# Kernel tuning notes

Measured on AMD Instinct MI355X. Metric: run time of the kernel, lower is better.

The kernel has to match this reference:

```python
import jax, jax.numpy as jnp
import numpy as np

B, T, C = 16, 2048, 1024
HEAD = 64

def setup_inputs() -> dict:
    key = jax.random.key(0)
    kx, kq, kk, kv = jax.random.split(key, 4)
    x = jax.random.normal(kx, (B, T, C), dtype=jnp.float32)
    s = 1.0 / np.sqrt(C)
    Wq = jax.random.normal(kq, (C, HEAD), dtype=jnp.float32) * s
    Wk = jax.random.normal(kk, (C, HEAD), dtype=jnp.float32) * s
    Wv = jax.random.normal(kv, (C, HEAD), dtype=jnp.float32) * s
    return {"x": x, "Wq": Wq, "Wk": Wk, "Wv": Wv}

def reference(x, Wq, Wk, Wv):
    Bb, Tt, Cc = x.shape
    q = jnp.einsum('btc,ch->bth', x, Wq)  # [B,T,H]
    k = jnp.einsum('btc,ch->bth', x, Wk)
    v = jnp.einsum('btc,ch->bth', x, Wv)
    # NOTE: source scales by C**-0.5 (n_embd), not head_size**-0.5
    scores = jnp.einsum('bth,bsh->bts', q, k) * (Cc ** -0.5)  # [B,T,T]
    causal = jnp.tril(jnp.ones((Tt, Tt), dtype=bool))
    scores = jnp.where(causal, scores, -jnp.inf)
    attn = jax.nn.softmax(scores, axis=-1)  # dropout p=0 -> identity
    out = jnp.einsum('bts,bsh->bth', attn, v)  # [B,T,H]
    return out
```

## Files before the change

kernel.cpp:

```cpp
#include <hip/hip_runtime.h>

typedef __bf16 bf16;
typedef __bf16 bf16x4 __attribute__((ext_vector_type(4)));
typedef __bf16 bf16x8 __attribute__((ext_vector_type(8)));
typedef float f32x4 __attribute__((ext_vector_type(4)));

#define TT_ 2048
#define CC_ 1024
#define HH_ 64

#define SCALE2 0.045084221f

__global__ __launch_bounds__(256) void prep_w(const float* __restrict__ Wq,
                                              const float* __restrict__ Wk,
                                              const float* __restrict__ Wv,
                                              bf16* __restrict__ Wt) {
    __shared__ bf16 Ls[64 * 65];
    const int m  = blockIdx.x >> 4;
    const int k0 = (blockIdx.x & 15) * 64;
    const float* W = (m == 0) ? Wq : (m == 1) ? Wk : Wv;
    const int tid = threadIdx.x;
    #pragma unroll
    for (int j = 0; j < 4; ++j) {
        int idx = tid + 256 * j;
        int r   = idx >> 4;
        int c4  = (idx & 15) * 4;
        float4 w = *(const float4*)&W[(size_t)(k0 + r) * HH_ + c4];
        Ls[r * 65 + c4 + 0] = (bf16)w.x;
        Ls[r * 65 + c4 + 1] = (bf16)w.y;
        Ls[r * 65 + c4 + 2] = (bf16)w.z;
        Ls[r * 65 + c4 + 3] = (bf16)w.w;
    }
    __syncthreads();
    #pragma unroll
    for (int j = 0; j < 4; ++j) {
        int idx = tid + 256 * j;
        int n   = idx >> 4;
        int kc  = (idx & 15) * 4;
        bf16x4 v;
        #pragma unroll
        for (int i = 0; i < 4; ++i) v[i] = Ls[(kc + i) * 65 + n];
        *(bf16x4*)&Wt[m * 65536 + n * 1024 + k0 + kc] = v;
    }
}

__global__ __launch_bounds__(256) void qkv_kernel(const float* __restrict__ x,
                                                  const bf16* __restrict__ Wt,
                                                  bf16* __restrict__ qb,
                                                  bf16* __restrict__ kb,
                                                  bf16* __restrict__ vt) {
    __shared__ __align__(16) bf16 Xs[2][64 * 72];
    const int tid  = threadIdx.x;
    const int wave = tid >> 6;
    const int lane = tid & 15;
    const int quad = (tid & 63) >> 4;
    const int m0   = blockIdx.x * 64;

    f32x4 acc[4][3];
    #pragma unroll
    for (int i = 0; i < 4; ++i)
        #pragma unroll
        for (int j = 0; j < 3; ++j) acc[i][j] = f32x4{0.f, 0.f, 0.f, 0.f};

    const int srow = tid >> 4;
    const int scol = (tid & 15) * 4;

    float4 xr[4];
    #pragma unroll
    for (int rr = 0; rr < 4; ++rr)
        xr[rr] = *(const float4*)&x[(size_t)(m0 + srow + rr * 16) * CC_ + scol];
    #pragma unroll
    for (int rr = 0; rr < 4; ++rr) {
        bf16x4 bv = {(bf16)xr[rr].x, (bf16)xr[rr].y, (bf16)xr[rr].z, (bf16)xr[rr].w};
        *(bf16x4*)&Xs[0][(srow + rr * 16) * 72 + scol] = bv;
    }

    for (int kbi = 0; kbi < 16; ++kbi) {
        const int cur = kbi & 1;
        const int k0  = kbi * 64;
        __syncthreads();
        if (kbi < 15) {
            #pragma unroll
            for (int rr = 0; rr < 4; ++rr)
                xr[rr] = *(const float4*)&x[(size_t)(m0 + srow + rr * 16) * CC_ + k0 + 64 + scol];
        }
        bf16x8 bfr[2][3];
        #pragma unroll
        for (int step = 0; step < 2; ++step)
            #pragma unroll
            for (int ct = 0; ct < 3; ++ct)
                bfr[step][ct] = *(const bf16x8*)&Wt[(size_t)(wave * 48 + ct * 16 + lane) * 1024 + k0 + step * 32 + quad * 8];
        bf16x8 afr[2][4];
        #pragma unroll
        for (int step = 0; step < 2; ++step)
            #pragma unroll
            for (int rt = 0; rt < 4; ++rt)
                afr[step][rt] = *(const bf16x8*)&Xs[cur][(rt * 16 + lane) * 72 + step * 32 + quad * 8];
        #pragma unroll
        for (int step = 0; step < 2; ++step)
            #pragma unroll
            for (int ct = 0; ct < 3; ++ct)
                #pragma unroll
                for (int rt = 0; rt < 4; ++rt)
                    acc[rt][ct] = __builtin_amdgcn_mfma_f32_16x16x32_bf16(afr[step][rt], bfr[step][ct], acc[rt][ct], 0, 0, 0);
        if (kbi < 15) {
            #pragma unroll
            for (int rr = 0; rr < 4; ++rr) {
                bf16x4 bv = {(bf16)xr[rr].x, (bf16)xr[rr].y, (bf16)xr[rr].z, (bf16)xr[rr].w};
                *(bf16x4*)&Xs[cur ^ 1][(srow + rr * 16) * 72 + scol] = bv;
            }
        }
    }

    const int bb = m0 >> 11;
    const int t0 = m0 & 2047;
    __syncthreads();
    #pragma unroll
    for (int ct = 0; ct < 3; ++ct) {
        int c0 = wave * 48 + ct * 16;
        if (c0 < 128) {
            bf16* outp = (c0 < 64) ? qb : kb;
            int h = (c0 & 63) + lane;
            #pragma unroll
            for (int rt = 0; rt < 4; ++rt)
                #pragma unroll
                for (int r = 0; r < 4; ++r)
                    outp[(size_t)(m0 + rt * 16 + quad * 4 + r) * HH_ + h] = (bf16)acc[rt][ct][r];
        } else {
            int h = (c0 - 128) + lane;
            #pragma unroll
            for (int rt = 0; rt < 4; ++rt)
                #pragma unroll
                for (int r = 0; r < 4; ++r)
                    Xs[0][(rt * 16 + quad * 4 + r) * 72 + h] = (bf16)acc[rt][ct][r];
        }
    }
    __syncthreads();
    {
        int h  = tid >> 2;
        int tc = (tid & 3) * 16;
        bf16x8 v0, v1;
        #pragma unroll
        for (int i = 0; i < 8; ++i) v0[i] = Xs[0][(tc + i) * 72 + h];
        #pragma unroll
        for (int i = 0; i < 8; ++i) v1[i] = Xs[0][(tc + 8 + i) * 72 + h];
        bf16* dst = &vt[(size_t)bb * HH_ * TT_ + (size_t)h * TT_ + t0 + tc];
        *(bf16x8*)dst = v0;
        *(bf16x8*)(dst + 8) = v1;
    }
}

__global__ __launch_bounds__(256) void attn_kernel(const bf16* __restrict__ qb,
                                                   const bf16* __restrict__ kb,
                                                   const bf16* __restrict__ vt,
                                                   bf16* __restrict__ PO,
                                                   float* __restrict__ PL) {
    __shared__ __align__(16) bf16 Ks[128 * 72];
    __shared__ __align__(16) bf16 Vs[64 * 136];
    __shared__ __align__(16) bf16 Ps[4][16 * 136];

    const int tid  = threadIdx.x;
    const int wave = tid >> 6;
    const int lane = tid & 15;
    const int quad = (tid & 63) >> 4;
    const int idx = blockIdx.x;
    const int bb  = blockIdx.y;
    int seg, qi;
    if (idx < 32)      { seg = 0; qi = idx; }
    else if (idx < 56) { seg = 1; qi = idx - 24; }
    else if (idx < 72) { seg = 2; qi = idx - 40; }
    else               { seg = 3; qi = idx - 48; }
    const int q0   = qi * 64;
    const int qrow = q0 + wave * 16;
    const int nch   = (seg < (qi >> 3)) ? 4 : (((qi & 7) + 2) >> 1);
    const int diagc = (seg == (qi >> 3)) ? nch - 1 : -1;

    bf16x8 aq[2];
    #pragma unroll
    for (int step = 0; step < 2; ++step)
        aq[step] = *(const bf16x8*)&qb[(size_t)(bb * TT_ + qrow + lane) * HH_ + step * 32 + quad * 8];

    f32x4 o_acc[4];
    #pragma unroll
    for (int ht = 0; ht < 4; ++ht) o_acc[ht] = f32x4{0.f, 0.f, 0.f, 0.f};
    float l_lane[4] = {0.f, 0.f, 0.f, 0.f};

    for (int c = 0; c < nch; ++c) {
        const int s0 = seg * 512 + c * 128;
        __syncthreads();
        #pragma unroll
        for (int j = 0; j < 4; ++j) {
            int ch = tid + 256 * j;
            int row = ch >> 3, c8 = (ch & 7) * 8;
            *(bf16x8*)&Ks[row * 72 + c8] =
                *(const bf16x8*)&kb[(size_t)(bb * TT_ + s0 + row) * HH_ + c8];
        }
        #pragma unroll
        for (int j = 0; j < 4; ++j) {
            int ch = tid + 256 * j;
            int h = ch >> 4, c8 = (ch & 15) * 8;
            *(bf16x8*)&Vs[h * 136 + c8] =
                *(const bf16x8*)&vt[(size_t)bb * HH_ * TT_ + (size_t)h * TT_ + s0 + c8];
        }
        __syncthreads();

        f32x4 sfr[8];
        #pragma unroll
        for (int nt = 0; nt < 8; ++nt) sfr[nt] = f32x4{0.f, 0.f, 0.f, 0.f};
        #pragma unroll
        for (int step = 0; step < 2; ++step)
            #pragma unroll
            for (int nt = 0; nt < 8; ++nt) {
                bf16x8 bk = *(const bf16x8*)&Ks[(nt * 16 + lane) * 72 + step * 32 + quad * 8];
                sfr[nt] = __builtin_amdgcn_mfma_f32_16x16x32_bf16(aq[step], bk, sfr[nt], 0, 0, 0);
            }

        const bool msk = (c == diagc);
        #pragma unroll
        for (int r = 0; r < 4; ++r) {
            const int rowg = qrow + quad * 4 + r;
            #pragma unroll
            for (int nt = 0; nt < 8; ++nt) {
                float e = __builtin_amdgcn_exp2f(sfr[nt][r] * SCALE2);
                if (msk && (s0 + nt * 16 + lane) > rowg) e = 0.f;
                sfr[nt][r] = e;
                l_lane[r] += e;
            }
        }

        #pragma unroll
        for (int nt = 0; nt < 8; ++nt)
            #pragma unroll
            for (int r = 0; r < 4; ++r)
                Ps[wave][(quad * 4 + r) * 136 + nt * 16 + lane] = (bf16)sfr[nt][r];

        #pragma unroll
        for (int step = 0; step < 4; ++step) {
            bf16x8 ap = *(const bf16x8*)&Ps[wave][lane * 136 + step * 32 + quad * 8];
            #pragma unroll
            for (int ht = 0; ht < 4; ++ht) {
                bf16x8 bv = *(const bf16x8*)&Vs[(ht * 16 + lane) * 136 + step * 32 + quad * 8];
                o_acc[ht] = __builtin_amdgcn_mfma_f32_16x16x32_bf16(ap, bv, o_acc[ht], 0, 0, 0);
            }
        }
    }

    const size_t p = (size_t)bb * 80 + idx;
    #pragma unroll
    for (int ht = 0; ht < 4; ++ht)
        #pragma unroll
        for (int r = 0; r < 4; ++r)
            PO[p * 4096 + (size_t)(wave * 16 + quad * 4 + r) * 64 + ht * 16 + lane] = (bf16)o_acc[ht][r];
    #pragma unroll
    for (int r = 0; r < 4; ++r) {
        float l = l_lane[r];
        l += __shfl_xor(l, 1);
        l += __shfl_xor(l, 2);
        l += __shfl_xor(l, 4);
        l += __shfl_xor(l, 8);
        if (lane == 0) PL[p * 64 + wave * 16 + quad * 4 + r] = l;
    }
}

__global__ __launch_bounds__(256) void combine_kernel(const bf16* __restrict__ PO,
                                                      const float* __restrict__ PL,
                                                      float* __restrict__ out) {
    const int qi = blockIdx.x, bb = blockIdx.y;
    const int tid = threadIdx.x;
    const int r  = tid >> 2;
    const int cb = (tid & 3) * 16;
    const int ns = (qi >> 3) + 1;
    const int off[4] = {0, 32, 56, 72};

    float acc[16];
    #pragma unroll
    for (int i = 0; i < 16; ++i) acc[i] = 0.f;
    float l = 0.f;
    for (int s = 0; s < ns; ++s) {
        const size_t p = (size_t)bb * 80 + off[s] + qi - 8 * s;
        l += PL[p * 64 + r];
        const bf16* po = &PO[p * 4096 + (size_t)r * 64 + cb];
        bf16x8 a0 = *(const bf16x8*)po;
        bf16x8 a1 = *(const bf16x8*)(po + 8);
        #pragma unroll
        for (int i = 0; i < 8; ++i) { acc[i] += (float)a0[i]; acc[8 + i] += (float)a1[i]; }
    }
    const float inv = 1.0f / l;
    float* dst = &out[(size_t)(bb * TT_ + qi * 64 + r) * HH_ + cb];
    #pragma unroll
    for (int v = 0; v < 4; ++v) {
        float4 o = {acc[v * 4] * inv, acc[v * 4 + 1] * inv, acc[v * 4 + 2] * inv, acc[v * 4 + 3] * inv};
        *(float4*)(dst + v * 4) = o;
    }
}

extern "C" void kernel_launch(void* const* d_in, const int* in_sizes, int n_in,
                              void* d_out, int out_size, void* d_ws, size_t ws_size,
                              hipStream_t stream) {
    const float* x  = (const float*)d_in[0];
    const float* Wq = (const float*)d_in[1];
    const float* Wk = (const float*)d_in[2];
    const float* Wv = (const float*)d_in[3];
    float* out = (float*)d_out;

    char* ws = (char*)d_ws;
    bf16*  qb = (bf16*)(ws);
    bf16*  kb = (bf16*)(ws + 4194304);
    bf16*  vt = (bf16*)(ws + 8388608);
    bf16*  Wt = (bf16*)(ws + 12582912);
    bf16*  PO = (bf16*)(ws + 12976128);
    float* PL = (float*)(ws + 23461888);

    prep_w<<<48, 256, 0, stream>>>(Wq, Wk, Wv, Wt);
    qkv_kernel<<<512, 256, 0, stream>>>(x, Wt, qb, kb, vt);
    attn_kernel<<<dim3(80, 16), 256, 0, stream>>>(qb, kb, vt, PO, PL);
    combine_kernel<<<dim3(32, 16), 256, 0, stream>>>(PO, PL, out);
}
```

Measured before the change: 259.8 us.

## Keep softmax probabilities in registers via transposed QK^T and 16x16x16 MFMA for PV

The attention kernel now computes S^T (K as the A operand, Q as B), so each lane's accumulator layout matches the A-operand layout of a 16x16x16 bf16 MFMA. The exponentiated scores can then feed the PV product directly from registers, with no Ps shared-memory round trip. K is read straight from global memory instead of being staged in LDS. V is double-buffered in LDS with register prefetch so there is one barrier per chunk, and fully masked diagonal sub-tiles are skipped. Risks are more global K traffic per wave, lower MFMA K-depth for PV, and the launch-bounds hint of 4 blocks per SM possibly constraining registers.

After: 272.1 us. 1.05x slower.

```diff
diff --git a/kernel.cpp b/kernel.cpp
--- a/kernel.cpp
+++ b/kernel.cpp
@@ -4,12 +4,27 @@
 typedef __bf16 bf16x4 __attribute__((ext_vector_type(4)));
 typedef __bf16 bf16x8 __attribute__((ext_vector_type(8)));
 typedef float f32x4 __attribute__((ext_vector_type(4)));
+typedef short short4v __attribute__((ext_vector_type(4)));
 
 #define TT_ 2048
 #define CC_ 1024
 #define HH_ 64
 
 #define SCALE2 0.045084221f
+
+static __device__ __forceinline__ f32x4 mfma16x16x16(bf16x4 a, bf16x4 b, f32x4 c) {
+#if __has_builtin(__builtin_amdgcn_mfma_f32_16x16x16_bf16)
+    return __builtin_amdgcn_mfma_f32_16x16x16_bf16(a, b, c, 0, 0, 0);
+#elif __has_builtin(__builtin_amdgcn_mfma_f32_16x16x16bf16_1k)
+    return __builtin_amdgcn_mfma_f32_16x16x16bf16_1k(__builtin_bit_cast(short4v, a),
+                                                     __builtin_bit_cast(short4v, b),
+                                                     c, 0, 0, 0);
+#else
+    f32x4 d;
+    asm("v_mfma_f32_16x16x16_bf16 %0, %1, %2, %3" : "=v"(d) : "v"(a), "v"(b), "v"(c));
+    return d;
+#endif
+}
 
 __global__ __launch_bounds__(256) void prep_w(const float* __restrict__ Wq,
                                               const float* __restrict__ Wk,
@@ -150,14 +165,12 @@
     }
 }
 
-__global__ __launch_bounds__(256) void attn_kernel(const bf16* __restrict__ qb,
-                                                   const bf16* __restrict__ kb,
-                                                   const bf16* __restrict__ vt,
-                                                   bf16* __restrict__ PO,
-                                                   float* __restrict__ PL) {
-    __shared__ __align__(16) bf16 Ks[128 * 72];
-    __shared__ __align__(16) bf16 Vs[64 * 136];
-    __shared__ __align__(16) bf16 Ps[4][16 * 136];
+__global__ __launch_bounds__(256, 4) void attn_kernel(const bf16* __restrict__ qb,
+                                                      const bf16* __restrict__ kb,
+                                                      const bf16* __restrict__ vt,
+                                                      bf16* __restrict__ PO,
+                                                      float* __restrict__ PL) {
+    __shared__ __align__(16) bf16 Vs[2][64 * 136];
 
     const int tid  = threadIdx.x;
     const int wave = tid >> 6;
@@ -170,78 +183,92 @@
     else if (idx < 56) { seg = 1; qi = idx - 24; }
     else if (idx < 72) { seg = 2; qi = idx - 40; }
     else               { seg = 3; qi = idx - 48; }
-    const int q0   = qi * 64;
-    const int qrow = q0 + wave * 16;
+    const int q0    = qi * 64;
     const int nch   = (seg < (qi >> 3)) ? 4 : (((qi & 7) + 2) >> 1);
     const int diagc = (seg == (qi >> 3)) ? nch - 1 : -1;
+    const int s00   = seg * 512;
+
+    const int qrow  = q0 + wave * 16;
+    const int qg    = qrow + lane;
+    const int qmaxw = qrow + 15;
 
     bf16x8 aq[2];
     #pragma unroll
     for (int step = 0; step < 2; ++step)
-        aq[step] = *(const bf16x8*)&qb[(size_t)(bb * TT_ + qrow + lane) * HH_ + step * 32 + quad * 8];
+        aq[step] = *(const bf16x8*)&qb[(size_t)(bb * TT_ + qg) * HH_ + step * 32 + quad * 8];
+
+    const bf16* kbase = kb + (size_t)(bb * TT_ + s00 + lane) * HH_ + quad * 8;
+
+    const int h0 = tid >> 4;
+    const int c8 = (tid & 15) * 8;
+    const bf16* vsrc = vt + (size_t)bb * HH_ * TT_ + (size_t)h0 * TT_ + c8;
+
+    bf16x8 vr[4];
+    #pragma unroll
+    for (int j = 0; j < 4; ++j) vr[j] = *(const bf16x8*)&vsrc[s00 + j * 16 * TT_];
+    #pragma unroll
+    for (int j = 0; j < 4; ++j) *(bf16x8*)&Vs[0][(h0 + 16 * j) * 136 + c8] = vr[j];
+    __syncthreads();
 
     f32x4 o_acc[4];
     #pragma unroll
     for (int ht = 0; ht < 4; ++ht) o_acc[ht] = f32x4{0.f, 0.f, 0.f, 0.f};
-    float l_lane[4] = {0.f, 0.f, 0.f, 0.f};
+    float lsum = 0.f;
 
     for (int c = 0; c < nch; ++c) {
-        const int s0 = seg * 512 + c * 128;
-        __syncthreads();
-        #pragma unroll
-        for (int j = 0; j < 4; ++j) {
-            int ch = tid + 256 * j;
-            int row = ch >> 3, c8 = (ch & 7) * 8;
-            *(bf16x8*)&Ks[row * 72 + c8] =
-                *(const bf16x8*)&kb[(size_t)(bb * TT_ + s0 + row) * HH_ + c8];
-        }
-        #pragma unroll
-        for (int j = 0; j < 4; ++j) {
-            int ch = tid + 256 * j;
-            int h = ch >> 4, c8 = (ch & 15) * 8;
-            *(bf16x8*)&Vs[h * 136 + c8] =
-                *(const bf16x8*)&vt[(size_t)bb * HH_ * TT_ + (size_t)h * TT_ + s0 + c8];
-        }
-        __syncthreads();
+        const int s0 = s00 + c * 128;
+        const bf16* Vcur = &Vs[c & 1][0];
+        const bool msk = (c == diagc);
+
+        if (c + 1 < nch) {
+            #pragma unroll
+            for (int j = 0; j < 4; ++j)
+                vr[j] = *(const bf16x8*)&vsrc[s0 + 128 + j * 16 * TT_];
+        }
 
         f32x4 sfr[8];
         #pragma unroll
-        for (int nt = 0; nt < 8; ++nt) sfr[nt] = f32x4{0.f, 0.f, 0.f, 0.f};
-        #pragma unroll
-        for (int step = 0; step < 2; ++step)
-            #pragma unroll
-            for (int nt = 0; nt < 8; ++nt) {
-                bf16x8 bk = *(const bf16x8*)&Ks[(nt * 16 + lane) * 72 + step * 32 + quad * 8];
-                sfr[nt] = __builtin_amdgcn_mfma_f32_16x16x32_bf16(aq[step], bk, sfr[nt], 0, 0, 0);
+        for (int nt = 0; nt < 8; ++nt) {
+            if (!msk || (s0 + nt * 16 <= qmaxw)) {
+                bf16x8 ak0 = *(const bf16x8*)&kbase[(c * 128 + nt * 16) * HH_];
+                bf16x8 ak1 = *(const bf16x8*)&kbase[(c * 128 + nt * 16) * HH_ + 32];
+                f32x4 s = f32x4{0.f, 0.f, 0.f, 0.f};
+                s = __builtin_amdgcn_mfma_f32_16x16x32_bf16(ak0, aq[0], s, 0, 0, 0);
+                s = __builtin_amdgcn_mfma_f32_16x16x32_bf16(ak1, aq[1], s, 0, 0, 0);
+                sfr[nt] = s;
             }
-
-        const bool msk = (c == diagc);
-        #pragma unroll
-        for (int r = 0; r < 4; ++r) {
-            const int rowg = qrow + quad * 4 + r;
-            #pragma unroll
-            for (int nt = 0; nt < 8; ++nt) {
-                float e = __builtin_amdgcn_exp2f(sfr[nt][r] * SCALE2);
-                if (msk && (s0 + nt * 16 + lane) > rowg) e = 0.f;
-                sfr[nt][r] = e;
-                l_lane[r] += e;
+        }
+
+        #pragma unroll
+        for (int nt = 0; nt < 8; ++nt) {
+            if (!msk || (s0 + nt * 16 <= qmaxw)) {
+                const int kb0 = s0 + nt * 16 + quad * 4;
+                f32x4 s = sfr[nt];
+                float e0 = __builtin_amdgcn_exp2f(s[0] * SCALE2);
+                float e1 = __builtin_amdgcn_exp2f(s[1] * SCALE2);
+                float e2 = __builtin_amdgcn_exp2f(s[2] * SCALE2);
+                float e3 = __builtin_amdgcn_exp2f(s[3] * SCALE2);
+                if (msk) {
+                    if (kb0 + 0 > qg) e0 = 0.f;
+                    if (kb0 + 1 > qg) e1 = 0.f;
+                    if (kb0 + 2 > qg) e2 = 0.f;
+                    if (kb0 + 3 > qg) e3 = 0.f;
+                }
+                lsum += (e0 + e1) + (e2 + e3);
+                bf16x4 ap = {(bf16)e0, (bf16)e1, (bf16)e2, (bf16)e3};
+                #pragma unroll
+                for (int ht = 0; ht < 4; ++ht) {
+                    bf16x4 bv = *(const bf16x4*)&Vcur[(ht * 16 + lane) * 136 + nt * 16 + quad * 4];
+                    o_acc[ht] = mfma16x16x16(ap, bv, o_acc[ht]);
+                }
             }
         }
 
-        #pragma unroll
-        for (int nt = 0; nt < 8; ++nt)
-            #pragma unroll
-            for (int r = 0; r < 4; ++r)
-                Ps[wave][(quad * 4 + r) * 136 + nt * 16 + lane] = (bf16)sfr[nt][r];
-
-        #pragma unroll
-        for (int step = 0; step < 4; ++step) {
-            bf16x8 ap = *(const bf16x8*)&Ps[wave][lane * 136 + step * 32 + quad * 8];
-            #pragma unroll
-            for (int ht = 0; ht < 4; ++ht) {
-                bf16x8 bv = *(const bf16x8*)&Vs[(ht * 16 + lane) * 136 + step * 32 + quad * 8];
-                o_acc[ht] = __builtin_amdgcn_mfma_f32_16x16x32_bf16(ap, bv, o_acc[ht], 0, 0, 0);
-            }
+        if (c + 1 < nch) {
+            #pragma unroll
+            for (int j = 0; j < 4; ++j)
+                *(bf16x8*)&Vs[(c + 1) & 1][(h0 + 16 * j) * 136 + c8] = vr[j];
+            __syncthreads();
         }
     }
 
@@ -251,15 +278,11 @@
         #pragma unroll
         for (int r = 0; r < 4; ++r)
             PO[p * 4096 + (size_t)(wave * 16 + quad * 4 + r) * 64 + ht * 16 + lane] = (bf16)o_acc[ht][r];
-    #pragma unroll
-    for (int r = 0; r < 4; ++r) {
-        float l = l_lane[r];
-        l += __shfl_xor(l, 1);
-        l += __shfl_xor(l, 2);
-        l += __shfl_xor(l, 4);
-        l += __shfl_xor(l, 8);
-        if (lane == 0) PL[p * 64 + wave * 16 + quad * 4 + r] = l;
-    }
+
+    float l = lsum;
+    l += __shfl_xor(l, 16);
+    l += __shfl_xor(l, 32);
+    if (quad == 0) PL[p * 64 + wave * 16 + lane] = l;
 }
 
 __global__ __launch_bounds__(256) void combine_kernel(const bf16* __restrict__ PO,
```

## Compute transposed S tiles and pass P to PV MFMA via permlane swaps

Applied to the files above, without the earlier changes.

Swaps the MFMA operands so the score tile comes out transposed (keys by queries). The exponentiated probabilities are then packed to bf16 and rearranged in registers with v_permlane32/16_swap into the A-operand layout for the PV MFMA. This removes the per-wave LDS P buffer round trip and skips fully masked 16-key sub-tiles on the diagonal chunk. It also simplifies the row-sum reduction and adds a launch bound minimum of 4 blocks, at the cost of more register-shuffle logic and reliance on the gfx950 permlane swap instructions.

Result: faster. 244.5 us (-5.9%).

```diff
diff --git a/kernel.cpp b/kernel.cpp
--- a/kernel.cpp
+++ b/kernel.cpp
@@ -1,6 +1,7 @@
 #include <hip/hip_runtime.h>
 
 typedef __bf16 bf16;
+typedef __bf16 bf16x2 __attribute__((ext_vector_type(2)));
 typedef __bf16 bf16x4 __attribute__((ext_vector_type(4)));
 typedef __bf16 bf16x8 __attribute__((ext_vector_type(8)));
 typedef float f32x4 __attribute__((ext_vector_type(4)));
@@ -10,6 +11,18 @@
 #define HH_ 64
 
 #define SCALE2 0.045084221f
+
+static __device__ __forceinline__ unsigned pack_bf16(float a, float b) {
+    union { bf16x2 h; unsigned u; } z;
+    z.h = bf16x2{(bf16)a, (bf16)b};
+    return z.u;
+}
+static __device__ __forceinline__ void plswap32(unsigned &a, unsigned &b) {
+    asm("v_permlane32_swap_b32 %0, %1" : "+v"(a), "+v"(b));
+}
+static __device__ __forceinline__ void plswap16(unsigned &a, unsigned &b) {
+    asm("v_permlane16_swap_b32 %0, %1" : "+v"(a), "+v"(b));
+}
 
 __global__ __launch_bounds__(256) void prep_w(const float* __restrict__ Wq,
                                               const float* __restrict__ Wk,
@@ -150,14 +163,13 @@
     }
 }
 
-__global__ __launch_bounds__(256) void attn_kernel(const bf16* __restrict__ qb,
-                                                   const bf16* __restrict__ kb,
-                                                   const bf16* __restrict__ vt,
-                                                   bf16* __restrict__ PO,
-                                                   float* __restrict__ PL) {
+__global__ __launch_bounds__(256, 4) void attn_kernel(const bf16* __restrict__ qb,
+                                                      const bf16* __restrict__ kb,
+                                                      const bf16* __restrict__ vt,
+                                                      bf16* __restrict__ PO,
+                                                      float* __restrict__ PL) {
     __shared__ __align__(16) bf16 Ks[128 * 72];
     __shared__ __align__(16) bf16 Vs[64 * 136];
-    __shared__ __align__(16) bf16 Ps[4][16 * 136];
 
     const int tid  = threadIdx.x;
     const int wave = tid >> 6;
@@ -170,23 +182,27 @@
     else if (idx < 56) { seg = 1; qi = idx - 24; }
     else if (idx < 72) { seg = 2; qi = idx - 40; }
     else               { seg = 3; qi = idx - 48; }
-    const int q0   = qi * 64;
-    const int qrow = q0 + wave * 16;
+    const int q0    = qi * 64;
     const int nch   = (seg < (qi >> 3)) ? 4 : (((qi & 7) + 2) >> 1);
     const int diagc = (seg == (qi >> 3)) ? nch - 1 : -1;
+    const int s00   = seg * 512;
+
+    const int qrow  = q0 + wave * 16;
+    const int qg    = qrow + lane;
+    const int qmaxw = qrow + 15;
 
     bf16x8 aq[2];
     #pragma unroll
     for (int step = 0; step < 2; ++step)
-        aq[step] = *(const bf16x8*)&qb[(size_t)(bb * TT_ + qrow + lane) * HH_ + step * 32 + quad * 8];
+        aq[step] = *(const bf16x8*)&qb[(size_t)(bb * TT_ + qg) * HH_ + step * 32 + quad * 8];
 
     f32x4 o_acc[4];
     #pragma unroll
     for (int ht = 0; ht < 4; ++ht) o_acc[ht] = f32x4{0.f, 0.f, 0.f, 0.f};
-    float l_lane[4] = {0.f, 0.f, 0.f, 0.f};
+    float lsum = 0.f;
 
     for (int c = 0; c < nch; ++c) {
-        const int s0 = seg * 512 + c * 128;
+        const int s0 = s00 + c * 128;
         __syncthreads();
         #pragma unroll
         for (int j = 0; j < 4; ++j) {
@@ -204,43 +220,64 @@
         }
         __syncthreads();
 
-        f32x4 sfr[8];
-        #pragma unroll
-        for (int nt = 0; nt < 8; ++nt) sfr[nt] = f32x4{0.f, 0.f, 0.f, 0.f};
-        #pragma unroll
-        for (int step = 0; step < 2; ++step)
-            #pragma unroll
-            for (int nt = 0; nt < 8; ++nt) {
-                bf16x8 bk = *(const bf16x8*)&Ks[(nt * 16 + lane) * 72 + step * 32 + quad * 8];
-                sfr[nt] = __builtin_amdgcn_mfma_f32_16x16x32_bf16(aq[step], bk, sfr[nt], 0, 0, 0);
-            }
-
         const bool msk = (c == diagc);
         #pragma unroll
-        for (int r = 0; r < 4; ++r) {
-            const int rowg = qrow + quad * 4 + r;
-            #pragma unroll
-            for (int nt = 0; nt < 8; ++nt) {
-                float e = __builtin_amdgcn_exp2f(sfr[nt][r] * SCALE2);
-                if (msk && (s0 + nt * 16 + lane) > rowg) e = 0.f;
-                sfr[nt][r] = e;
-                l_lane[r] += e;
-            }
-        }
-
-        #pragma unroll
-        for (int nt = 0; nt < 8; ++nt)
-            #pragma unroll
-            for (int r = 0; r < 4; ++r)
-                Ps[wave][(quad * 4 + r) * 136 + nt * 16 + lane] = (bf16)sfr[nt][r];
-
-        #pragma unroll
-        for (int step = 0; step < 4; ++step) {
-            bf16x8 ap = *(const bf16x8*)&Ps[wave][lane * 136 + step * 32 + quad * 8];
+        for (int w = 0; w < 4; ++w) {
+            if (msk && (s0 + w * 32 > qmaxw)) continue;
+            const bool haveB = !msk || (s0 + w * 32 + 16 <= qmaxw);
+
+            f32x4 sA = {0.f, 0.f, 0.f, 0.f};
+            f32x4 sB = {0.f, 0.f, 0.f, 0.f};
+            {
+                bf16x8 ak0 = *(const bf16x8*)&Ks[(w * 32 + lane) * 72 + quad * 8];
+                bf16x8 ak1 = *(const bf16x8*)&Ks[(w * 32 + lane) * 72 + 32 + quad * 8];
+                sA = __builtin_amdgcn_mfma_f32_16x16x32_bf16(ak0, aq[0], sA, 0, 0, 0);
+                sA = __builtin_amdgcn_mfma_f32_16x16x32_bf16(ak1, aq[1], sA, 0, 0, 0);
+            }
+            if (haveB) {
+                bf16x8 bk0 = *(const bf16x8*)&Ks[(w * 32 + 16 + lane) * 72 + quad * 8];
+                bf16x8 bk1 = *(const bf16x8*)&Ks[(w * 32 + 16 + lane) * 72 + 32 + quad * 8];
+                sB = __builtin_amdgcn_mfma_f32_16x16x32_bf16(bk0, aq[0], sB, 0, 0, 0);
+                sB = __builtin_amdgcn_mfma_f32_16x16x32_bf16(bk1, aq[1], sB, 0, 0, 0);
+            }
+
+            const int kA0 = s0 + w * 32 + quad * 4;
+            float eA[4], eB[4];
+            #pragma unroll
+            for (int r = 0; r < 4; ++r) {
+                float e = __builtin_amdgcn_exp2f(sA[r] * SCALE2);
+                if (msk && (kA0 + r > qg)) e = 0.f;
+                eA[r] = e;
+            }
+            if (haveB) {
+                #pragma unroll
+                for (int r = 0; r < 4; ++r) {
+                    float e = __builtin_amdgcn_exp2f(sB[r] * SCALE2);
+                    if (msk && (kA0 + 16 + r > qg)) e = 0.f;
+                    eB[r] = e;
+                }
+            } else {
+                #pragma unroll
+                for (int r = 0; r < 4; ++r) eB[r] = 0.f;
+            }
+            lsum += ((eA[0] + eA[1]) + (eA[2] + eA[3])) +
+                    ((eB[0] + eB[1]) + (eB[2] + eB[3]));
+
+            unsigned d0 = pack_bf16(eA[0], eA[1]);
+            unsigned d1 = pack_bf16(eA[2], eA[3]);
+            unsigned d2 = pack_bf16(eB[0], eB[1]);
+            unsigned d3 = pack_bf16(eB[2], eB[3]);
+            plswap32(d0, d2);
+            plswap16(d0, d2);
+            plswap32(d1, d3);
+            plswap16(d1, d3);
+            union { unsigned u[4]; bf16x8 v; } apu;
+            apu.u[0] = d0; apu.u[1] = d1; apu.u[2] = d2; apu.u[3] = d3;
+
             #pragma unroll
             for (int ht = 0; ht < 4; ++ht) {
-                bf16x8 bv = *(const bf16x8*)&Vs[(ht * 16 + lane) * 136 + step * 32 + quad * 8];
-                o_acc[ht] = __builtin_amdgcn_mfma_f32_16x16x32_bf16(ap, bv, o_acc[ht], 0, 0, 0);
+                bf16x8 bv = *(const bf16x8*)&Vs[(ht * 16 + lane) * 136 + w * 32 + quad * 8];
+                o_acc[ht] = __builtin_amdgcn_mfma_f32_16x16x32_bf16(apu.v, bv, o_acc[ht], 0, 0, 0);
             }
         }
     }
@@ -251,15 +288,11 @@
         #pragma unroll
         for (int r = 0; r < 4; ++r)
             PO[p * 4096 + (size_t)(wave * 16 + quad * 4 + r) * 64 + ht * 16 + lane] = (bf16)o_acc[ht][r];
-    #pragma unroll
-    for (int r = 0; r < 4; ++r) {
-        float l = l_lane[r];
-        l += __shfl_xor(l, 1);
-        l += __shfl_xor(l, 2);
-        l += __shfl_xor(l, 4);
-        l += __shfl_xor(l, 8);
-        if (lane == 0) PL[p * 64 + wave * 16 + quad * 4 + r] = l;
-    }
+
+    float l = lsum;
+    l += __shfl_xor(l, 16);
+    l += __shfl_xor(l, 32);
+    if (quad == 0) PL[p * 64 + wave * 16 + lane] = l;
 }
 
 __global__ __launch_bounds__(256) void combine_kernel(const bf16* __restrict__ PO,
```
